# Optimization experiments

Measured on AMD Instinct MI355X. Metric: run time of the kernel, lower is better.

Reference implementation:

```python
import jax, jax.numpy as jnp
import numpy as np

D_MODEL = 1024
N_HEADS = 16
HEAD_DIM = D_MODEL // N_HEADS
NEG_INF = -1e30


def _rotary(v):
    # v: [B, H, T, hd]. Original module rotates each (even, odd) pair by 90 deg:
    # out[..., 2i] = -v[..., 2i+1]; out[..., 2i+1] = v[..., 2i]
    v2 = v.reshape(*v.shape[:-1], HEAD_DIM // 2, 2)
    return jnp.stack([-v2[..., 1], v2[..., 0]], axis=-1).reshape(v.shape)


def setup_inputs() -> dict:
    key = jax.random.key(0)
    ks = jax.random.split(key, 9)
    B, T, D = 2, 2048, D_MODEL
    s = 1.0 / np.sqrt(D)
    inp = {
        "x": jax.random.normal(ks[0], (B, T, D), dtype=jnp.float32),
        "Wq_w": jax.random.normal(ks[1], (D, D), dtype=jnp.float32) * s,
        "Wq_b": jnp.zeros((D,), dtype=jnp.float32),
        "Wk_w": jax.random.normal(ks[2], (D, D), dtype=jnp.float32) * s,
        "Wk_b": jnp.zeros((D,), dtype=jnp.float32),
        "Wv_w": jax.random.normal(ks[3], (D, D), dtype=jnp.float32) * s,
        "Wv_b": jnp.zeros((D,), dtype=jnp.float32),
        "Wo_w": jax.random.normal(ks[4], (D, D), dtype=jnp.float32) * s,
        "Wo_b": jnp.zeros((D,), dtype=jnp.float32),
    }
    # create_sparse_mask: block-diagonal True windows of size T//4
    window = T // 4
    blk = jnp.arange(T) // window
    inp["sparse_mask"] = blk[:, None] == blk[None, :]
    return inp


def reference(x, Wq_w, Wq_b, Wk_w, Wk_b, Wv_w, Wv_b, Wo_w, Wo_b, sparse_mask):
    B, T, D = x.shape
    H, hd = N_HEADS, HEAD_DIM

    def proj(w, b):  # [B,T,D] -> [B,H,T,hd]
        return (x @ w.T + b).reshape(B, T, H, hd).transpose(0, 2, 1, 3)

    q = _rotary(proj(Wq_w, Wq_b))
    k = _rotary(proj(Wk_w, Wk_b))
    v = proj(Wv_w, Wv_b)

    scores = jnp.einsum("bhqd,bhkd->bhqk", q, k) / jnp.sqrt(jnp.asarray(hd, x.dtype))
    causal = jnp.tril(jnp.ones((T, T), dtype=bool))
    allowed = sparse_mask & causal  # block-diagonal AND causal
    scores = jnp.where(allowed, scores, NEG_INF)
    attn = jax.nn.softmax(scores, axis=-1)  # dropout_p=0.1 omitted (eval mode)
    out = jnp.einsum("bhqk,bhkd->bhqd", attn, v)
    out = out.transpose(0, 2, 1, 3).reshape(B, T, D)
    return out @ Wo_w.T + Wo_b
```

## Files before the change

### kernel.cpp

```cpp
#include <hip/hip_runtime.h>
#include <hip/hip_bf16.h>
#include <stdint.h>

typedef __attribute__((ext_vector_type(4))) float f32x4;
typedef __attribute__((ext_vector_type(8))) __bf16 bf16x8;
typedef __attribute__((ext_vector_type(4))) unsigned short u16x4;
typedef __attribute__((ext_vector_type(8))) unsigned short u16x8;
typedef __attribute__((ext_vector_type(2))) unsigned int u32x2;
typedef const __attribute__((address_space(1))) void* as1_cvp;
typedef __attribute__((address_space(3))) void* as3_vp;

#define LOG2E 1.44269504088896340736f

#define VMW0() asm volatile("s_waitcnt vmcnt(0)" ::: "memory")
#define VMW2() asm volatile("s_waitcnt vmcnt(2)" ::: "memory")
#define BAR()  do { __builtin_amdgcn_sched_barrier(0); __builtin_amdgcn_s_barrier(); \
                    __builtin_amdgcn_sched_barrier(0); } while (0)

static __device__ __forceinline__ unsigned short f2bf(float f) {
  union { float f; unsigned int u; } c; c.f = f;
  unsigned int r = c.u + 0x7FFFu + ((c.u >> 16) & 1u);
  return (unsigned short)(r >> 16);
}

static __device__ __forceinline__ void gl_lds16(const void* g, void* l) {
  __builtin_amdgcn_global_load_lds((as1_cvp)(uintptr_t)g, (as3_vp)(uintptr_t)l, 16, 0, 0);
}

__global__ __launch_bounds__(256) void cvt_kernel(
    const float* __restrict__ x, const float* __restrict__ wq, const float* __restrict__ wk,
    const float* __restrict__ wv, const float* __restrict__ wo,
    unsigned short* __restrict__ xb, unsigned short* __restrict__ wqb,
    unsigned short* __restrict__ wkb, unsigned short* __restrict__ wvb,
    unsigned short* __restrict__ wob) {
  long e = ((long)blockIdx.x * 256 + threadIdx.x) * 8;
  const float* s; unsigned short* d; long o;
  if (e < 4194304)      { s = x;  d = xb;  o = e; }
  else if (e < 5242880) { s = wq; d = wqb; o = e - 4194304; }
  else if (e < 6291456) { s = wk; d = wkb; o = e - 5242880; }
  else if (e < 7340032) { s = wv; d = wvb; o = e - 6291456; }
  else                  { s = wo; d = wob; o = e - 7340032; }
  float4 a = *(const float4*)(s + o);
  float4 b = *(const float4*)(s + o + 4);
  u16x8 v;
  v[0] = f2bf(a.x); v[1] = f2bf(a.y); v[2] = f2bf(a.z); v[3] = f2bf(a.w);
  v[4] = f2bf(b.x); v[5] = f2bf(b.y); v[6] = f2bf(b.z); v[7] = f2bf(b.w);
  *(u16x8*)(d + o) = v;
}

__global__ __launch_bounds__(512, 4) void gemm_qkv8(
    const unsigned short* __restrict__ xb, const unsigned short* __restrict__ wcat,
    const float* __restrict__ bq, const float* __restrict__ bk, const float* __restrict__ bv,
    unsigned short* __restrict__ qo, unsigned short* __restrict__ ko,
    unsigned short* __restrict__ vto) {
  __shared__ __align__(16) char lds[81920];
  const int tid = threadIdx.x;
  const int lane = tid & 63, wid = tid >> 6;
  const int wm = wid >> 2, wn = wid & 3;
  const int c = lane & 15, g = lane >> 4;

  const int bid = blockIdx.x;
  const int xcd = bid & 7, idx = bid >> 3;
  const int m0 = (((xcd >> 1) << 3) + (idx >> 3)) << 7;
  const int n0 = (((xcd & 1) << 3) + (idx & 7)) * 192;

  const int srow = tid >> 3;
  const int coff = (((tid & 7) ^ (srow & 7)) << 4);
  const char* Ab = (const char*)xb;
  const char* Bb = (const char*)wcat;

  const int swzr0 = ((g ^ (c & 7)) << 4);
  const int swzr1 = (((4 | g) ^ (c & 7)) << 4);

  f32x4 acc[4][3] = {};

  auto STAGE = [&](int kt, int unit) {
    char* db = lds + (kt & 1) * 40960;
    const char* gp; char* dst;
    if (unit < 2) {
      gp = Ab + ((long)(m0 + unit * 64 + srow) << 11) + (kt << 7) + coff;
      dst = db + unit * 8192 + tid * 16;
    } else {
      gp = Bb + ((long)(n0 + (unit - 2) * 64 + srow) << 11) + (kt << 7) + coff;
      dst = db + 16384 + (unit - 2) * 8192 + tid * 16;
    }
    gl_lds16(gp, dst);
  };

#pragma unroll
  for (int uu = 0; uu < 5; ++uu) STAGE(0, uu);
  VMW0();
  BAR();

#pragma unroll 1
  for (int kt = 0; kt < 16; ++kt) {
    const int bufb = (kt & 1) * 40960;
    if (kt < 15) {
#pragma unroll
      for (int uu = 0; uu < 5; ++uu) STAGE(kt + 1, uu);
    }
    bf16x8 aa[4][2];
    const char* pA = lds + bufb + (wm << 13) + (c << 7);
#pragma unroll
    for (int f = 0; f < 4; ++f) {
      aa[f][0] = *(const bf16x8*)(pA + (f << 11) + swzr0);
      aa[f][1] = *(const bf16x8*)(pA + (f << 11) + swzr1);
    }
#pragma unroll
    for (int nf = 0; nf < 3; ++nf) {
      const int rB = wn * 48 + (nf << 4) + c;
      const char* pB = lds + bufb + 16384 + ((rB >> 6) << 13) + ((rB & 63) << 7);
      bf16x8 b0 = *(const bf16x8*)(pB + swzr0);
      bf16x8 b1 = *(const bf16x8*)(pB + swzr1);
      __builtin_amdgcn_s_setprio(1);
#pragma unroll
      for (int f = 0; f < 4; ++f)
        acc[f][nf] = __builtin_amdgcn_mfma_f32_16x16x32_bf16(aa[f][0], b0, acc[f][nf], 0, 0, 0);
#pragma unroll
      for (int f = 0; f < 4; ++f)
        acc[f][nf] = __builtin_amdgcn_mfma_f32_16x16x32_bf16(aa[f][1], b1, acc[f][nf], 0, 0, 0);
      __builtin_amdgcn_s_setprio(0);
    }
    if (kt < 15) VMW0();
    BAR();
  }

#pragma unroll
  for (int nf = 0; nf < 3; ++nf) {
    const int n = n0 + wn * 48 + (nf << 4) + c;
    const int z = n >> 10, nn = n & 1023;
    const float bb_ = (z == 0 ? bq : z == 1 ? bk : bv)[nn];
    const float sc = (z == 0) ? 0.125f : 1.0f;
    const int h = nn >> 6, dd = nn & 63;
#pragma unroll
    for (int a = 0; a < 4; ++a) {
      const int mb = m0 + (wm << 6) + (a << 4) + (g << 2);
      const int b = mb >> 11, tt = mb & 2047;
      if (z < 2) {
        unsigned short* dst = (z == 0 ? qo : ko) +
            ((((long)(b << 4) + h) << 11) + tt) * 64 + dd;
#pragma unroll
        for (int j = 0; j < 4; ++j) dst[(long)j * 64] = f2bf((acc[a][nf][j] + bb_) * sc);
      } else {
        u16x4 pk;
#pragma unroll
        for (int j = 0; j < 4; ++j) pk[j] = f2bf(acc[a][nf][j] + bb_);
        *(u16x4*)(vto + ((((long)((b << 4) + h) << 6) + dd) << 11) + tt) = pk;
      }
    }
  }
}

__global__ __launch_bounds__(512, 4) void gemm_oproj8(
    const unsigned short* __restrict__ ab, const unsigned short* __restrict__ wob,
    const float* __restrict__ bo, float* __restrict__ out) {
  __shared__ __align__(16) char lds[49152];
  const int tid = threadIdx.x;
  const int lane = tid & 63, wid = tid >> 6;
  const int wm = wid >> 2, wn = wid & 3;
  const int c = lane & 15, g = lane >> 4;

  const int bid = blockIdx.x;
  const int xcd = bid & 7, idx = bid >> 3;
  const int m0 = ((xcd << 3) + (idx >> 3)) << 6;
  const int n0 = (idx & 7) << 7;

  const int srow = tid >> 3;
  const int coff = (((tid & 7) ^ (srow & 7)) << 4);
  const char* Ab = (const char*)ab;
  const char* Bb = (const char*)wob;

  const int swzr0 = ((g ^ (c & 7)) << 4);
  const int swzr1 = (((4 | g) ^ (c & 7)) << 4);

  f32x4 acc[2][2] = {};

  auto STAGE = [&](int kt, int unit) {
    char* db = lds + (kt & 1) * 24576;
    const char* gp; char* dst;
    if (unit == 0) {
      gp = Ab + ((long)(m0 + srow) << 11) + (kt << 7) + coff;
      dst = db + tid * 16;
    } else {
      gp = Bb + ((long)(n0 + (unit - 1) * 64 + srow) << 11) + (kt << 7) + coff;
      dst = db + unit * 8192 + tid * 16;
    }
    gl_lds16(gp, dst);
  };

  STAGE(0, 0); STAGE(0, 1); STAGE(0, 2);
  VMW0();
  BAR();

#pragma unroll 1
  for (int kt = 0; kt < 16; ++kt) {
    const int bufb = (kt & 1) * 24576;
    if (kt < 15) { STAGE(kt + 1, 0); STAGE(kt + 1, 1); STAGE(kt + 1, 2); }
    bf16x8 aa[2][2];
    const char* pA = lds + bufb + (wm << 12) + (c << 7);
#pragma unroll
    for (int f = 0; f < 2; ++f) {
      aa[f][0] = *(const bf16x8*)(pA + (f << 11) + swzr0);
      aa[f][1] = *(const bf16x8*)(pA + (f << 11) + swzr1);
    }
#pragma unroll
    for (int nf = 0; nf < 2; ++nf) {
      const int rB = (wn << 5) + (nf << 4) + c;
      const char* pB = lds + bufb + 8192 + ((rB >> 6) << 13) + ((rB & 63) << 7);
      bf16x8 b0 = *(const bf16x8*)(pB + swzr0);
      bf16x8 b1 = *(const bf16x8*)(pB + swzr1);
      __builtin_amdgcn_s_setprio(1);
#pragma unroll
      for (int f = 0; f < 2; ++f)
        acc[f][nf] = __builtin_amdgcn_mfma_f32_16x16x32_bf16(aa[f][0], b0, acc[f][nf], 0, 0, 0);
#pragma unroll
      for (int f = 0; f < 2; ++f)
        acc[f][nf] = __builtin_amdgcn_mfma_f32_16x16x32_bf16(aa[f][1], b1, acc[f][nf], 0, 0, 0);
      __builtin_amdgcn_s_setprio(0);
    }
    if (kt < 15) VMW0();
    BAR();
  }

#pragma unroll
  for (int nf = 0; nf < 2; ++nf) {
    const int n = n0 + (wn << 5) + (nf << 4) + c;
    const float bb = bo[n];
#pragma unroll
    for (int f = 0; f < 2; ++f) {
      const int mb = m0 + (wm << 5) + (f << 4) + (g << 2);
#pragma unroll
      for (int j = 0; j < 4; ++j)
        out[((long)(mb + j) << 10) + n] = acc[f][nf][j] + bb;
    }
  }
}

__global__ __launch_bounds__(512) void attn_kernel(
    const unsigned short* __restrict__ qg, const unsigned short* __restrict__ kg,
    const unsigned short* __restrict__ vtg, unsigned short* __restrict__ og) {
  __shared__ __align__(16) char kv_s[3][16384];
  __shared__ __align__(16) char p_s[8][2304];

  const int bx = blockIdx.x, bh = blockIdx.y;
  const int map1[16] = {3,7,11,15, 2,6,10,14, 0,4,8,12, 1,5,9,13};
  const int map2[16] = {0,4,8,12, 1,5,9,13, 3,7,11,15, 2,6,10,14};
  const int qt = (bh < 16) ? map1[bx] : map2[bx];
  const int tid = threadIdx.x;
  const int lane = tid & 63, w = tid >> 6;
  const int c = lane & 15, g = lane >> 4;
  const int q0 = qt << 7;
  const int wstart = q0 & ~511;
  const int nt = ((q0 - wstart) >> 6) + 2;

  const unsigned short* qrow = qg + (((long)bh << 11) + q0 + (w << 4) + c) * 64;
  bf16x8 qa0 = *(const bf16x8*)(qrow + (g << 3));
  bf16x8 qa1 = *(const bf16x8*)(qrow + (g << 3) + 32);

  float m_run = -3.0e38f, l_run = 0.0f;
  f32x4 oacc[4] = {};

  const int sr = tid >> 3;
  const int jx16 = (((tid & 7) ^ (sr & 7)) << 4);
  const char* kbase = (const char*)kg + ((((long)bh << 11) + sr) << 7) + jx16;
  const char* vbase = (const char*)vtg + ((((long)bh << 6) + sr) << 12) + jx16;
  const int t16 = tid << 4;

  auto STAGEKV = [&](int kv0, int bsel) {
    char* dst = kv_s[bsel];
    gl_lds16(kbase + ((long)kv0 << 7), dst + t16);
    gl_lds16(vbase + ((long)kv0 << 1), dst + 8192 + t16);
  };

  STAGEKV(wstart, 0);
  STAGEKV(wstart + 64, 1);

  int rsel = 0, ssel = 2;
  for (int t = 0; t < nt; ++t) {
    if (t + 1 < nt) VMW2(); else VMW0();
    BAR();

    const char* kb_ = kv_s[rsel];
    const char* vb_ = kv_s[rsel] + 8192;
    const int kv0 = wstart + (t << 6);

    f32x4 sacc[4] = {};
    __builtin_amdgcn_s_setprio(1);
#pragma unroll
    for (int mf = 0; mf < 4; ++mf) {
      const int kr = (mf << 4) + c;
      const char* kp = kb_ + (kr << 7);
      bf16x8 k0 = *(const bf16x8*)(kp + ((g ^ (kr & 7)) << 4));
      bf16x8 k1 = *(const bf16x8*)(kp + (((4 | g) ^ (kr & 7)) << 4));
      sacc[mf] = __builtin_amdgcn_mfma_f32_16x16x32_bf16(k0, qa0, sacc[mf], 0, 0, 0);
      sacc[mf] = __builtin_amdgcn_mfma_f32_16x16x32_bf16(k1, qa1, sacc[mf], 0, 0, 0);
    }
    __builtin_amdgcn_s_setprio(0);

    const int dkv = kv0 - q0;
    if (dkv > (w << 4) - 64) {
      const int qrel = (w << 4) + c;
#pragma unroll
      for (int mf = 0; mf < 4; ++mf)
#pragma unroll
        for (int j = 0; j < 4; ++j)
          if (dkv + (mf << 4) + (g << 2) + j > qrel) sacc[mf][j] = -3.0e38f;
    }

    float pm[4];
#pragma unroll
    for (int mf = 0; mf < 4; ++mf)
      pm[mf] = fmaxf(fmaxf(sacc[mf][0], sacc[mf][1]), fmaxf(sacc[mf][2], sacc[mf][3]));
    float pmax = fmaxf(fmaxf(pm[0], pm[1]), fmaxf(pm[2], pm[3]));
    pmax = fmaxf(pmax, __shfl_xor(pmax, 16));
    pmax = fmaxf(pmax, __shfl_xor(pmax, 32));

    const bool resc = !__all(pmax <= m_run + 8.0f);
    const float m_new = resc ? fmaxf(m_run, pmax) : m_run;

    const float mL = m_new * LOG2E;
    float ls[4];
#pragma unroll
    for (int mf = 0; mf < 4; ++mf) {
      float p0 = __builtin_amdgcn_exp2f(__builtin_fmaf(sacc[mf][0], LOG2E, -mL));
      float p1 = __builtin_amdgcn_exp2f(__builtin_fmaf(sacc[mf][1], LOG2E, -mL));
      float p2 = __builtin_amdgcn_exp2f(__builtin_fmaf(sacc[mf][2], LOG2E, -mL));
      float p3 = __builtin_amdgcn_exp2f(__builtin_fmaf(sacc[mf][3], LOG2E, -mL));
      sacc[mf][0] = p0; sacc[mf][1] = p1; sacc[mf][2] = p2; sacc[mf][3] = p3;
      ls[mf] = (p0 + p1) + (p2 + p3);
    }
    float lsum = (ls[0] + ls[1]) + (ls[2] + ls[3]);
    lsum += __shfl_xor(lsum, 16);
    lsum += __shfl_xor(lsum, 32);

    if (resc) {
      const float alpha = __builtin_amdgcn_exp2f((m_run - m_new) * LOG2E);
      l_run *= alpha;
#pragma unroll
      for (int j = 0; j < 4; ++j) {
        const float aj = __shfl(alpha, (g << 2) + j);
#pragma unroll
        for (int nf = 0; nf < 4; ++nf) oacc[nf][j] *= aj;
      }
      m_run = m_new;
    }
    l_run += lsum;

    {
      char* pw = p_s[w] + c * 144;
#pragma unroll
      for (int mf = 0; mf < 4; ++mf) {
        unsigned int p01, p23;
        asm("v_cvt_pk_bf16_f32 %0, %1, %2" : "=v"(p01) : "v"(sacc[mf][0]), "v"(sacc[mf][1]));
        asm("v_cvt_pk_bf16_f32 %0, %1, %2" : "=v"(p23) : "v"(sacc[mf][2]), "v"(sacc[mf][3]));
        u32x2 pk; pk[0] = p01; pk[1] = p23;
        *(u32x2*)(pw + (mf << 5) + (g << 3)) = pk;
      }
    }

    const char* pr = p_s[w] + c * 144;
    __builtin_amdgcn_s_setprio(1);
#pragma unroll
    for (int kk = 0; kk < 2; ++kk) {
      bf16x8 pa = *(const bf16x8*)(pr + (kk << 6) + (g << 4));
#pragma unroll
      for (int nf = 0; nf < 4; ++nf) {
        const int vr = (nf << 4) + c;
        bf16x8 vb = *(const bf16x8*)(vb_ + (vr << 7) +
                                     ((((kk << 2) | g) ^ (vr & 7)) << 4));
        oacc[nf] = __builtin_amdgcn_mfma_f32_16x16x32_bf16(pa, vb, oacc[nf], 0, 0, 0);
      }
    }
    __builtin_amdgcn_s_setprio(0);

    if (t + 2 < nt) STAGEKV(wstart + ((t + 2) << 6), ssel);

    rsel = (rsel == 2) ? 0 : rsel + 1;
    ssel = (ssel == 2) ? 0 : ssel + 1;
  }

  const int b = bh >> 4, h = bh & 15;
#pragma unroll
  for (int j = 0; j < 4; ++j) {
    const float linv = 1.0f / __shfl(l_run, (g << 2) + j);
    const int trow = q0 + (w << 4) + (g << 2) + j;
    unsigned short* dst = og + ((((long)(b << 11)) + trow) << 10) + (h << 6);
#pragma unroll
    for (int nf = 0; nf < 4; ++nf)
      dst[(nf << 4) + c] = f2bf(oacc[nf][j] * linv);
  }
}

extern "C" void kernel_launch(void* const* d_in, const int* in_sizes, int n_in,
                              void* d_out, int out_size, void* d_ws, size_t ws_size,
                              hipStream_t stream) {
  const float* x  = (const float*)d_in[0];
  const float* wq = (const float*)d_in[1];
  const float* bq = (const float*)d_in[2];
  const float* wk = (const float*)d_in[3];
  const float* bk = (const float*)d_in[4];
  const float* wv = (const float*)d_in[5];
  const float* bv = (const float*)d_in[6];
  const float* wo = (const float*)d_in[7];
  const float* bo = (const float*)d_in[8];

  char* ws = (char*)d_ws;
  unsigned short* xb    = (unsigned short*)(ws);
  unsigned short* wqb   = (unsigned short*)(ws + 8388608);
  unsigned short* wkb   = (unsigned short*)(ws + 10485760);
  unsigned short* wvb   = (unsigned short*)(ws + 12582912);
  unsigned short* wob   = (unsigned short*)(ws + 14680064);
  unsigned short* qb    = (unsigned short*)(ws + 16777216);
  unsigned short* kb    = (unsigned short*)(ws + 25165824);
  unsigned short* vtb   = (unsigned short*)(ws + 33554432);
  unsigned short* attnb = xb;

  cvt_kernel<<<4096, 256, 0, stream>>>(x, wq, wk, wv, wo, xb, wqb, wkb, wvb, wob);
  gemm_qkv8<<<512, 512, 0, stream>>>(xb, wqb, bq, bk, bv, qb, kb, vtb);
  attn_kernel<<<dim3(16, 32), 512, 0, stream>>>(qb, kb, vtb, attnb);
  gemm_oproj8<<<512, 512, 0, stream>>>(attnb, wob, bo, (float*)d_out);
}
```

Baseline: 70.98 us.

## Restructure QKV GEMM into 128x128 tiles with 5-slot, 4-deep async LDS pipeline

Result: slower. 77.44 us (+9.1%).

```diff
diff --git a/kernel.cpp b/kernel.cpp
--- a/kernel.cpp
+++ b/kernel.cpp
@@ -14,6 +14,8 @@
 
 #define VMW0() asm volatile("s_waitcnt vmcnt(0)" ::: "memory")
 #define VMW2() asm volatile("s_waitcnt vmcnt(2)" ::: "memory")
+#define VMW4() asm volatile("s_waitcnt vmcnt(4)" ::: "memory")
+#define VMW6() asm volatile("s_waitcnt vmcnt(6)" ::: "memory")
 #define BAR()  do { __builtin_amdgcn_sched_barrier(0); __builtin_amdgcn_s_barrier(); \
                     __builtin_amdgcn_sched_barrier(0); } while (0)
 
@@ -61,90 +63,81 @@
 
   const int bid = blockIdx.x;
   const int xcd = bid & 7, idx = bid >> 3;
-  const int m0 = (((xcd >> 1) << 3) + (idx >> 3)) << 7;
-  const int n0 = (((xcd & 1) << 3) + (idx & 7)) * 192;
-
-  const int srow = tid >> 3;
-  const int coff = (((tid & 7) ^ (srow & 7)) << 4);
+  const int m0 = (((xcd >> 1) << 3) + idx / 12) << 7;
+  const int n0 = (((xcd & 1) * 12) + idx % 12) << 7;
+
+  const int sj = tid >> 3;
+  const int sg = (tid & 7) ^ (sj & 7);
+  const long soff = (((long)(sj + ((sg >> 2) << 6))) << 11) + ((sg & 3) << 4);
   const char* Ab = (const char*)xb;
   const char* Bb = (const char*)wcat;
 
-  const int swzr0 = ((g ^ (c & 7)) << 4);
-  const int swzr1 = (((4 | g) ^ (c & 7)) << 4);
-
-  f32x4 acc[4][3] = {};
-
-  auto STAGE = [&](int kt, int unit) {
-    char* db = lds + (kt & 1) * 40960;
-    const char* gp; char* dst;
-    if (unit < 2) {
-      gp = Ab + ((long)(m0 + unit * 64 + srow) << 11) + (kt << 7) + coff;
-      dst = db + unit * 8192 + tid * 16;
-    } else {
-      gp = Bb + ((long)(n0 + (unit - 2) * 64 + srow) << 11) + (kt << 7) + coff;
-      dst = db + 16384 + (unit - 2) * 8192 + tid * 16;
-    }
-    gl_lds16(gp, dst);
+  const int sA = ((((wm << 2) | g) ^ (c & 7)) << 4);
+  const int sB = (((((wn >> 1) << 2) | g) ^ (c & 7)) << 4);
+  const char* pAr = lds + (c << 7) + sA;
+  const char* pBr = lds + 8192 + ((((wn & 1) << 5) + c) << 7) + sB;
+
+  f32x4 acc[4][2] = {};
+
+  auto STAGE = [&](int t, int slot) {
+    char* db = lds + slot * 16384;
+    const long ko = (long)t << 6;
+    gl_lds16(Ab + ((long)m0 << 11) + soff + ko, db + tid * 16);
+    gl_lds16(Bb + ((long)n0 << 11) + soff + ko, db + 8192 + tid * 16);
   };
 
-#pragma unroll
-  for (int uu = 0; uu < 5; ++uu) STAGE(0, uu);
-  VMW0();
-  BAR();
-
+  STAGE(0, 0); STAGE(1, 1); STAGE(2, 2); STAGE(3, 3);
+
+  int rs = 0, ss = 4;
 #pragma unroll 1
-  for (int kt = 0; kt < 16; ++kt) {
-    const int bufb = (kt & 1) * 40960;
-    if (kt < 15) {
-#pragma unroll
-      for (int uu = 0; uu < 5; ++uu) STAGE(kt + 1, uu);
-    }
-    bf16x8 aa[4][2];
-    const char* pA = lds + bufb + (wm << 13) + (c << 7);
-#pragma unroll
-    for (int f = 0; f < 4; ++f) {
-      aa[f][0] = *(const bf16x8*)(pA + (f << 11) + swzr0);
-      aa[f][1] = *(const bf16x8*)(pA + (f << 11) + swzr1);
-    }
-#pragma unroll
-    for (int nf = 0; nf < 3; ++nf) {
-      const int rB = wn * 48 + (nf << 4) + c;
-      const char* pB = lds + bufb + 16384 + ((rB >> 6) << 13) + ((rB & 63) << 7);
-      bf16x8 b0 = *(const bf16x8*)(pB + swzr0);
-      bf16x8 b1 = *(const bf16x8*)(pB + swzr1);
-      __builtin_amdgcn_s_setprio(1);
-#pragma unroll
-      for (int f = 0; f < 4; ++f)
-        acc[f][nf] = __builtin_amdgcn_mfma_f32_16x16x32_bf16(aa[f][0], b0, acc[f][nf], 0, 0, 0);
-#pragma unroll
-      for (int f = 0; f < 4; ++f)
-        acc[f][nf] = __builtin_amdgcn_mfma_f32_16x16x32_bf16(aa[f][1], b1, acc[f][nf], 0, 0, 0);
-      __builtin_amdgcn_s_setprio(0);
-    }
-    if (kt < 15) VMW0();
+  for (int t = 0; t < 32; ++t) {
+    if (t <= 28) { VMW6(); }
+    else if (t == 29) { VMW4(); }
+    else if (t == 30) { VMW2(); }
+    else { VMW0(); }
     BAR();
-  }
-
-#pragma unroll
-  for (int nf = 0; nf < 3; ++nf) {
-    const int n = n0 + wn * 48 + (nf << 4) + c;
+
+    const int sb = rs * 16384;
+    bf16x8 aa[4];
+#pragma unroll
+    for (int f = 0; f < 4; ++f) aa[f] = *(const bf16x8*)(pAr + sb + (f << 11));
+    bf16x8 bb0 = *(const bf16x8*)(pBr + sb);
+    bf16x8 bb1 = *(const bf16x8*)(pBr + sb + 2048);
+    __builtin_amdgcn_s_setprio(1);
+#pragma unroll
+    for (int f = 0; f < 4; ++f)
+      acc[f][0] = __builtin_amdgcn_mfma_f32_16x16x32_bf16(aa[f], bb0, acc[f][0], 0, 0, 0);
+#pragma unroll
+    for (int f = 0; f < 4; ++f)
+      acc[f][1] = __builtin_amdgcn_mfma_f32_16x16x32_bf16(aa[f], bb1, acc[f][1], 0, 0, 0);
+    __builtin_amdgcn_s_setprio(0);
+
+    if (t + 4 < 32) STAGE(t + 4, ss);
+
+    rs = (rs == 4) ? 0 : rs + 1;
+    ss = (ss == 4) ? 0 : ss + 1;
+  }
+
+#pragma unroll
+  for (int nf = 0; nf < 2; ++nf) {
+    const int n = n0 + (wn << 5) + (nf << 4) + c;
     const int z = n >> 10, nn = n & 1023;
     const float bb_ = (z == 0 ? bq : z == 1 ? bk : bv)[nn];
     const float sc = (z == 0) ? 0.125f : 1.0f;
     const int h = nn >> 6, dd = nn & 63;
 #pragma unroll
-    for (int a = 0; a < 4; ++a) {
-      const int mb = m0 + (wm << 6) + (a << 4) + (g << 2);
+    for (int f = 0; f < 4; ++f) {
+      const int mb = m0 + (wm << 6) + (f << 4) + (g << 2);
       const int b = mb >> 11, tt = mb & 2047;
       if (z < 2) {
         unsigned short* dst = (z == 0 ? qo : ko) +
             ((((long)(b << 4) + h) << 11) + tt) * 64 + dd;
 #pragma unroll
-        for (int j = 0; j < 4; ++j) dst[(long)j * 64] = f2bf((acc[a][nf][j] + bb_) * sc);
+        for (int j = 0; j < 4; ++j) dst[(long)j * 64] = f2bf((acc[f][nf][j] + bb_) * sc);
       } else {
         u16x4 pk;
 #pragma unroll
-        for (int j = 0; j < 4; ++j) pk[j] = f2bf(acc[a][nf][j] + bb_);
+        for (int j = 0; j < 4; ++j) pk[j] = f2bf(acc[f][nf][j] + bb_);
         *(u16x4*)(vto + ((((long)((b << 4) + h) << 6) + dd) << 11) + tt) = pk;
       }
     }
@@ -416,7 +409,7 @@
   unsigned short* attnb = xb;
 
   cvt_kernel<<<4096, 256, 0, stream>>>(x, wq, wk, wv, wo, xb, wqb, wkb, wvb, wob);
-  gemm_qkv8<<<512, 512, 0, stream>>>(xb, wqb, bq, bk, bv, qb, kb, vtb);
+  gemm_qkv8<<<768, 512, 0, stream>>>(xb, wqb, bq, bk, bv, qb, kb, vtb);
   attn_kernel<<<dim3(16, 32), 512, 0, stream>>>(qb, kb, vtb, attnb);
   gemm_oproj8<<<512, 512, 0, stream>>>(attnb, wob, bo, (float*)d_out);
 }
```
